# Kernel optimization log

Measured on AMD Instinct MI355X. Metric: run time of the kernel, lower is better.

Reference implementation:

```python
import jax, jax.numpy as jnp
import numpy as np

B, NC, NF, D = 4, 256, 768, 768
TOK_RATIO = 0.5
LN_EPS = 1e-5


def _linear(x, w, b):
    # w: [D_in, D_out]
    return x @ w + b


def _leaky(x):
    return jax.nn.leaky_relu(x, negative_slope=0.01)


def setup_inputs() -> dict:
    key = jax.random.key(0)
    ks = jax.random.split(key, 12)
    s = 1.0 / np.sqrt(D)
    inp = {
        "cls_tokens": jax.random.normal(ks[0], (B, NC, D), dtype=jnp.float32),
        "feats": jax.random.normal(ks[1], (B, NF, D), dtype=jnp.float32),
        "W_head_w": jax.random.uniform(ks[2], (D, D), minval=-s, maxval=s),
        "W_head_b": jax.random.uniform(ks[3], (D,), minval=-s, maxval=s),
        "W_tail_w": jax.random.uniform(ks[4], (D, D), minval=-s, maxval=s),
        "W_tail_b": jax.random.uniform(ks[5], (D,), minval=-s, maxval=s),
        "lin1_w": jax.random.uniform(ks[6], (D, D), minval=-s, maxval=s),
        "lin1_b": jax.random.uniform(ks[7], (D,), minval=-s, maxval=s),
        "lin2_w": jax.random.uniform(ks[8], (D, D), minval=-s, maxval=s),
        "lin2_b": jax.random.uniform(ks[9], (D,), minval=-s, maxval=s),
        "ln_w": jnp.ones((D,), dtype=jnp.float32),
        "ln_b": jnp.zeros((D,), dtype=jnp.float32),
    }
    return inp


def reference(cls_tokens, feats, W_head_w, W_head_b, W_tail_w, W_tail_b,
              lin1_w, lin1_b, lin2_w, lin2_b, ln_w, ln_b):
    topk = int(TOK_RATIO * NC)
    scale = D ** (-0.5)

    # feats is detached in the original (clone().detach())
    x = jnp.concatenate([cls_tokens, jax.lax.stop_gradient(feats)], axis=1)  # [B, Nt, D]

    e_h = _linear(cls_tokens, W_head_w, W_head_b)  # [B, Nc, D]
    e_t = _linear(x, W_tail_w, W_tail_b)           # [B, Nt, D]

    attn_logit = jnp.einsum('bnd,bmd->bnm', e_h * scale, e_t)  # [B, Nc, Nt]
    topk_weight, topk_index = jax.lax.top_k(attn_logit, topk)  # [B, Nc, k]

    # Gather neighbor embeddings: Nb_h[b, n, j] = e_t[b, topk_index[b, n, j]]
    Nb_h = jax.vmap(lambda et, idx: et[idx])(e_t, topk_index)  # [B, Nc, k, D]

    topk_prob = jax.nn.softmax(topk_weight, axis=2)            # [B, Nc, k]
    p = topk_prob[..., None]
    eh_r = p * Nb_h + (1.0 - p) * e_h[:, :, None, :]           # [B, Nc, k, D]

    gate = jnp.tanh(e_h[:, :, None, :] + eh_r)
    ka_weight = jnp.einsum('bnkd,bnkd->bnk', Nb_h, gate)
    ka_prob = jax.nn.softmax(ka_weight, axis=2)
    e_Nh = jnp.einsum('bnk,bnkd->bnd', ka_prob, Nb_h)          # [B, Nc, D]

    # bi-interaction aggregation
    sum_emb = _leaky(_linear((e_h + e_Nh) * 0.1 + cls_tokens, lin1_w, lin1_b))
    bi_emb = _leaky(_linear(e_h * e_Nh * 0.1 + cls_tokens, lin2_w, lin2_b))
    embedding = sum_emb + bi_emb

    # LayerNorm (dropout is a no-op: p=0 and output overwritten in original)
    mu = jnp.mean(embedding, axis=-1, keepdims=True)
    var = jnp.var(embedding, axis=-1, keepdims=True)
    h = (embedding - mu) * jax.lax.rsqrt(var + LN_EPS) * ln_w + ln_b
    return h
```

## Files before the change

kernel.cpp:

```cpp
#include <hip/hip_runtime.h>
#include <hip/hip_bf16.h>
#include <math.h>

#define DDIM 768
#define NCLS 256
#define NFEAT 768
#define NTOK 1024
#define NBATCH 4
#define KSEL 128

typedef float f32x4 __attribute__((ext_vector_type(4)));
typedef short s16x8 __attribute__((ext_vector_type(8)));

__device__ __forceinline__ float wsum(float v) {
#pragma unroll
  for (int o = 32; o; o >>= 1) v += __shfl_down(v, o, 64);
  return v;
}
__device__ __forceinline__ float wmaxr(float v) {
#pragma unroll
  for (int o = 32; o; o >>= 1) v = fmaxf(v, __shfl_down(v, o, 64));
  return v;
}
__device__ __forceinline__ short f2bf(float f) {
  union { __hip_bfloat16 h; short s; } u;
  u.h = __float2bfloat16(f);
  return u.s;
}
__device__ __forceinline__ float bf2f(short s) {
  union { unsigned u; float f; } c;
  c.u = ((unsigned)(unsigned short)s) << 16;
  return c.f;
}
__device__ __forceinline__ void cvt8(float4 x, float4 y, s16x8& h, s16x8& l) {
  float v[8] = {x.x, x.y, x.z, x.w, y.x, y.y, y.z, y.w};
#pragma unroll
  for (int i = 0; i < 8; ++i) {
    short hh = f2bf(v[i]);
    h[i] = hh;
    l[i] = f2bf(v[i] - bf2f(hh));
  }
}
__device__ __forceinline__ int swz(int row, int chunk) {
  return (row << 5) + (((chunk ^ (row >> 1)) & 3) << 3);
}

__global__ __launch_bounds__(256) void prep_all(
    const float* __restrict__ cls, const float* __restrict__ feats,
    const float* __restrict__ w0, const float* __restrict__ w1,
    const float* __restrict__ w2, const float* __restrict__ w3,
    short* __restrict__ h0, short* __restrict__ h1, short* __restrict__ h2,
    short* __restrict__ h3, short* __restrict__ l0, short* __restrict__ l1,
    short* __restrict__ Xh, short* __restrict__ Xl) {
  __shared__ float tile[32][33];
  const int bid = blockIdx.x;
  const int t = threadIdx.x;
  if (bid < 2304) {
    const int z = bid / 576, rem = bid % 576;
    const int by = rem / 24, bx = rem % 24;
    const float* s = z == 0 ? w0 : z == 1 ? w1 : z == 2 ? w2 : w3;
    short* dh = z == 0 ? h0 : z == 1 ? h1 : z == 2 ? h2 : h3;
    short* dl = z == 0 ? l0 : z == 1 ? l1 : nullptr;
    const int tx = t & 31, ty0 = t >> 5;
    const int r0 = by * 32, c0 = bx * 32;
#pragma unroll
    for (int i = 0; i < 4; ++i) {
      int ty = ty0 + i * 8;
      tile[ty][tx] = s[(size_t)(r0 + ty) * DDIM + c0 + tx];
    }
    __syncthreads();
#pragma unroll
    for (int i = 0; i < 4; ++i) {
      int ty = ty0 + i * 8;
      float v = tile[tx][ty];
      short hh = f2bf(v);
      dh[(size_t)(c0 + ty) * DDIM + r0 + tx] = hh;
      if (dl) dl[(size_t)(c0 + ty) * DDIM + r0 + tx] = f2bf(v - bf2f(hh));
    }
  } else {
    const size_t base = ((size_t)(bid - 2304) * 256 + t) * 8;
    const int row = (int)(base / DDIM);
    const int col = (int)(base % DDIM);
    const int b = row >> 10, rr = row & 1023;
    const float* src =
        (rr < NCLS) ? cls + ((size_t)b * NCLS + rr) * DDIM + col
                    : feats + ((size_t)b * NFEAT + (rr - NCLS)) * DDIM + col;
    float4 a0 = *(const float4*)(src);
    float4 a1 = *(const float4*)(src + 4);
    s16x8 h, l;
    cvt8(a0, a1, h, l);
    *(s16x8*)(Xh + base) = h;
    *(s16x8*)(Xl + base) = l;
  }
}

__global__ __launch_bounds__(256) void gemm_front(
    const short* __restrict__ Xh, const short* __restrict__ Xl,
    const short* __restrict__ WhT_h, const short* __restrict__ WhT_l,
    const float* __restrict__ Whb, const short* __restrict__ WtT_h,
    const short* __restrict__ WtT_l, const float* __restrict__ Wtb,
    short* __restrict__ eh_hi, short* __restrict__ eh_lo,
    short* __restrict__ et_hi, short* __restrict__ et_lo) {
  __shared__ short Ah[128 * 32], Al[128 * 32];
  __shared__ short Bh[64 * 32], Bl[64 * 32];
  const int bid = blockIdx.x;
  const int xcd = bid & 7, idx = bid >> 3;
  const int ytile = xcd * 5 + idx / 12;
  const int xtile = idx % 12;
  const int t = threadIdx.x;
  const int row0 = ytile * 128, col0 = xtile * 64;
  const bool head = row0 < 1024;

  const int ar = t >> 1, ac = (t & 1) * 2;
  const int aw0 = swz(ar, ac), aw1 = swz(ar, ac + 1);
  size_t xrow;
  {
    int gr = row0 + ar;
    xrow = head ? (size_t)(((gr >> 8) << 10) + (gr & 255)) : (size_t)(gr - 1024);
  }
  const short* aph = Xh + xrow * DDIM + ac * 8;
  const short* apl = Xl + xrow * DDIM + ac * 8;
  const int br = t >> 2, bc = t & 3;
  const int bw0 = swz(br, bc);
  const short* bph = (head ? WhT_h : WtT_h) + (size_t)(col0 + br) * DDIM + bc * 8;
  const short* bpl = (head ? WhT_l : WtT_l) + (size_t)(col0 + br) * DDIM + bc * 8;
  const float* biasu = head ? Whb : Wtb;

  const int lane = t & 63, wave = t >> 6;
  const int wr = wave >> 1, wc = wave & 1;
  const int fr = lane & 15, fq = lane >> 4;

  f32x4 acc[4][2] = {};
  s16x8 rah0 = *(const s16x8*)(aph);
  s16x8 rah1 = *(const s16x8*)(aph + 8);
  s16x8 ral0 = *(const s16x8*)(apl);
  s16x8 ral1 = *(const s16x8*)(apl + 8);
  s16x8 rbh = *(const s16x8*)(bph);
  s16x8 rbl = *(const s16x8*)(bpl);

  for (int kt = 0; kt < 24; ++kt) {
    __syncthreads();
    *(s16x8*)&Ah[aw0] = rah0;
    *(s16x8*)&Ah[aw1] = rah1;
    *(s16x8*)&Al[aw0] = ral0;
    *(s16x8*)&Al[aw1] = ral1;
    *(s16x8*)&Bh[bw0] = rbh;
    *(s16x8*)&Bl[bw0] = rbl;
    __syncthreads();
    const int kn = (kt < 23 ? kt + 1 : 23) * 32;
    rah0 = *(const s16x8*)(aph + kn);
    rah1 = *(const s16x8*)(aph + kn + 8);
    ral0 = *(const s16x8*)(apl + kn);
    ral1 = *(const s16x8*)(apl + kn + 8);
    rbh = *(const s16x8*)(bph + kn);
    rbl = *(const s16x8*)(bpl + kn);

    s16x8 afh[4], afl[4];
#pragma unroll
    for (int m = 0; m < 4; ++m) {
      int ao = swz(wr * 64 + m * 16 + fr, fq);
      afh[m] = *(const s16x8*)&Ah[ao];
      afl[m] = *(const s16x8*)&Al[ao];
    }
#pragma unroll
    for (int n = 0; n < 2; ++n) {
      int bo = swz(wc * 32 + n * 16 + fr, fq);
      s16x8 bfh = *(const s16x8*)&Bh[bo];
      s16x8 bfl = *(const s16x8*)&Bl[bo];
#pragma unroll
      for (int m = 0; m < 4; ++m) {
        acc[m][n] =
            __builtin_amdgcn_mfma_f32_16x16x32_bf16(afh[m], bfh, acc[m][n], 0, 0, 0);
        acc[m][n] =
            __builtin_amdgcn_mfma_f32_16x16x32_bf16(afh[m], bfl, acc[m][n], 0, 0, 0);
        acc[m][n] =
            __builtin_amdgcn_mfma_f32_16x16x32_bf16(afl[m], bfh, acc[m][n], 0, 0, 0);
      }
    }
  }

  short* Ch = head ? eh_hi : et_hi;
  short* Cl = head ? eh_lo : et_lo;
  const int rbase = head ? row0 : row0 - 1024;
#pragma unroll
  for (int m = 0; m < 4; ++m) {
#pragma unroll
    for (int n = 0; n < 2; ++n) {
#pragma unroll
      for (int r = 0; r < 4; ++r) {
        int rg = rbase + wr * 64 + m * 16 + fq * 4 + r;
        int cg = col0 + wc * 32 + n * 16 + fr;
        float v = acc[m][n][r] + biasu[cg];
        size_t o = (size_t)rg * DDIM + cg;
        short hh = f2bf(v);
        Ch[o] = hh;
        Cl[o] = f2bf(v - bf2f(hh));
      }
    }
  }
}

__global__ __launch_bounds__(256) void gemm_logits(
    const short* __restrict__ eh_hi, const short* __restrict__ eh_lo,
    const short* __restrict__ et_hi, const short* __restrict__ et_lo,
    float* __restrict__ logits, float scale) {
  __shared__ short Ah[32 * 32], Al[32 * 32];
  __shared__ short Bh[64 * 32], Bl[64 * 32];
  const int bid = blockIdx.x;
  const int xcd = bid & 7, idx = bid >> 3;
  const int batch = xcd >> 1;
  const int sub = ((xcd & 1) << 6) | idx;
  const int xtile = sub & 15, ytile = sub >> 4;
  const int row0 = ytile * 32, col0 = xtile * 64;
  const int t = threadIdx.x;

  const int ahalf = t >> 7, ac2 = t & 127;
  const int asr = ac2 >> 2, acc_ = ac2 & 3;
  const short* aptr = (ahalf ? eh_lo : eh_hi) +
                      ((size_t)batch * NCLS + row0 + asr) * DDIM + acc_ * 8;
  const int aso = swz(asr, acc_);
  const int bsr = t >> 2, bcc = t & 3;
  const short* bph = et_hi + ((size_t)batch * NTOK + col0 + bsr) * DDIM + bcc * 8;
  const short* bpl = et_lo + ((size_t)batch * NTOK + col0 + bsr) * DDIM + bcc * 8;
  const int bso = swz(bsr, bcc);

  const int lane = t & 63, wave = t >> 6;
  const int wr = wave >> 1, wc = wave & 1;
  const int fr = lane & 15, fq = lane >> 4;

  f32x4 acc[2] = {};
  s16x8 rA = *(const s16x8*)(aptr);
  s16x8 rbh = *(const s16x8*)(bph);
  s16x8 rbl = *(const s16x8*)(bpl);

  for (int kt = 0; kt < 24; ++kt) {
    __syncthreads();
    *(s16x8*)&(ahalf ? Al : Ah)[aso] = rA;
    *(s16x8*)&Bh[bso] = rbh;
    *(s16x8*)&Bl[bso] = rbl;
    __syncthreads();
    const int kn = (kt < 23 ? kt + 1 : 23) * 32;
    rA = *(const s16x8*)(aptr + kn);
    rbh = *(const s16x8*)(bph + kn);
    rbl = *(const s16x8*)(bpl + kn);
    int ao = swz(wr * 16 + fr, fq);
    s16x8 afh = *(const s16x8*)&Ah[ao];
    s16x8 afl = *(const s16x8*)&Al[ao];
#pragma unroll
    for (int n = 0; n < 2; ++n) {
      int bo = swz(wc * 32 + n * 16 + fr, fq);
      s16x8 bfh = *(const s16x8*)&Bh[bo];
      s16x8 bfl = *(const s16x8*)&Bl[bo];
      acc[n] = __builtin_amdgcn_mfma_f32_16x16x32_bf16(afh, bfh, acc[n], 0, 0, 0);
      acc[n] = __builtin_amdgcn_mfma_f32_16x16x32_bf16(afh, bfl, acc[n], 0, 0, 0);
      acc[n] = __builtin_amdgcn_mfma_f32_16x16x32_bf16(afl, bfh, acc[n], 0, 0, 0);
    }
  }

  float* Cb = logits + (size_t)batch * NCLS * NTOK;
#pragma unroll
  for (int n = 0; n < 2; ++n)
#pragma unroll
    for (int r = 0; r < 4; ++r) {
      int rg = row0 + wr * 16 + fq * 4 + r;
      int cg = col0 + wc * 32 + n * 16 + fr;
      Cb[(size_t)rg * NTOK + cg] = scale * acc[n][r];
    }
}

__global__ __launch_bounds__(256) void select_agg(
    const float* __restrict__ logits, const short* __restrict__ eh_hi,
    const short* __restrict__ et_hi, const float* __restrict__ cls,
    short* __restrict__ inbf) {
  const int bid = blockIdx.x;
  const int xcd = bid & 7, slot = bid >> 3;
  const int batch = xcd >> 1;
  const int row = batch * 256 + (xcd & 1) * 128 + slot;
  const int t = threadIdx.x, lane = t & 63, wave = t >> 6;

  __shared__ int hist[256];
  __shared__ int sh_bin, sh_rem;
  __shared__ int cnt;
  __shared__ int wsumT[4];
  __shared__ float p_sh[KSEL];
  __shared__ int idx_sh[KSEL];
  __shared__ float kaw_sh[KSEL];
  __shared__ float red[2];

  float4 v4 = *(const float4*)(logits + (size_t)row * NTOK + 4 * t);
  float val[4] = {v4.x, v4.y, v4.z, v4.w};
  unsigned key[4];
#pragma unroll
  for (int i = 0; i < 4; ++i) {
    unsigned u = __float_as_uint(val[i]);
    key[i] = (u & 0x80000000u) ? ~u : (u | 0x80000000u);
  }
  unsigned pref = 0, mask = 0;
  int rem = KSEL;
#pragma unroll
  for (int shift = 24; shift >= 0; shift -= 8) {
    hist[t] = 0;
    __syncthreads();
#pragma unroll
    for (int i = 0; i < 4; ++i)
      if ((key[i] & mask) == pref)
        atomicAdd(&hist[(key[i] >> shift) & 255], 1);
    __syncthreads();
    if (wave == 0) {
      int h0 = hist[4 * lane], h1 = hist[4 * lane + 1];
      int h2 = hist[4 * lane + 2], h3 = hist[4 * lane + 3];
      int s = h0 + h1 + h2 + h3;
#pragma unroll
      for (int o = 1; o < 64; o <<= 1) {
        int v = __shfl_down(s, o, 64);
        if (lane + o < 64) s += v;
      }
      int abv = __shfl_down(s, 1, 64);
      if (lane == 63) abv = 0;
      int c3 = abv + h3, c2 = c3 + h2, c1 = c2 + h1, c0 = c1 + h0;
      int bin = -1, nab = 0;
      if (c3 >= rem && abv < rem) { bin = 4 * lane + 3; nab = abv; }
      else if (c2 >= rem && c3 < rem) { bin = 4 * lane + 2; nab = c3; }
      else if (c1 >= rem && c2 < rem) { bin = 4 * lane + 1; nab = c2; }
      else if (c0 >= rem && c1 < rem) { bin = 4 * lane + 0; nab = c1; }
      if (bin >= 0) { sh_bin = bin; sh_rem = rem - nab; }
    }
    __syncthreads();
    pref |= ((unsigned)sh_bin) << shift;
    mask |= 0xFFu << shift;
    rem = sh_rem;
  }
  const unsigned T = pref;
  const int above = KSEL - rem;

  if (t == 0) cnt = 0;
  int tc = 0;
#pragma unroll
  for (int i = 0; i < 4; ++i) tc += (key[i] == T);
  int inc = tc;
#pragma unroll
  for (int o = 1; o < 64; o <<= 1) {
    int v = __shfl_up(inc, o, 64);
    if (lane >= o) inc += v;
  }
  if (lane == 63) wsumT[wave] = inc;
  __syncthreads();
  int wbase = 0;
#pragma unroll
  for (int w = 0; w < 4; ++w)
    if (w < wave) wbase += wsumT[w];
  int excl = wbase + inc - tc;
#pragma unroll
  for (int i = 0; i < 4; ++i) {
    if (key[i] > T) {
      int s2 = atomicAdd(&cnt, 1);
      p_sh[s2] = val[i];
      idx_sh[s2] = 4 * t + i;
    } else if (key[i] == T) {
      int r = excl++;
      if (r < rem) {
        p_sh[above + r] = val[i];
        idx_sh[above + r] = 4 * t + i;
      }
    }
  }
  __syncthreads();

  if (wave == 0) {
    float m = wmaxr(fmaxf(p_sh[lane], p_sh[lane + 64]));
    if (!lane) red[0] = m;
  }
  __syncthreads();
  if (t < KSEL) p_sh[t] = __expf(p_sh[t] - red[0]);
  __syncthreads();
  if (wave == 0) {
    float s = wsum(p_sh[lane] + p_sh[lane + 64]);
    if (!lane) red[1] = s;
  }
  __syncthreads();
  if (t < KSEL) p_sh[t] *= (1.f / red[1]);
  __syncthreads();

  float ehr[12];
  {
    const short* ehrow = eh_hi + (size_t)row * DDIM;
    s16x8 e8 = *(const s16x8*)(ehrow + 8 * lane);
    short4 e4 = *(const short4*)(ehrow + 512 + 4 * lane);
#pragma unroll
    for (int i = 0; i < 8; ++i) ehr[i] = bf2f(e8[i]);
    ehr[8] = bf2f(e4.x);
    ehr[9] = bf2f(e4.y);
    ehr[10] = bf2f(e4.z);
    ehr[11] = bf2f(e4.w);
  }
  const short* etb = et_hi + (size_t)batch * NTOK * DDIM;

  for (int i = 0; i < 32; ++i) {
    int j = wave * 32 + i;
    float pj = p_sh[j];
    float a = 4.f - 2.f * pj, b2 = 2.f * pj;
    const short* nb = etb + (size_t)idx_sh[j] * DDIM;
    s16x8 n8 = *(const s16x8*)(nb + 8 * lane);
    short4 n4 = *(const short4*)(nb + 512 + 4 * lane);
    float nq[12];
#pragma unroll
    for (int q = 0; q < 8; ++q) nq[q] = bf2f(n8[q]);
    nq[8] = bf2f(n4.x);
    nq[9] = bf2f(n4.y);
    nq[10] = bf2f(n4.z);
    nq[11] = bf2f(n4.w);
    float partial = 0.f;
#pragma unroll
    for (int q = 0; q < 12; ++q) {
      float y2 = fmaf(a, ehr[q], b2 * nq[q]);
      float ex = __expf(y2);
      float g = fmaf(-2.f, __builtin_amdgcn_rcpf(1.f + ex), 1.f);
      partial = fmaf(nq[q], g, partial);
    }
    partial = wsum(partial);
    if (!lane) kaw_sh[j] = partial;
  }
  __syncthreads();

  if (wave == 0) {
    float m = wmaxr(fmaxf(kaw_sh[lane], kaw_sh[lane + 64]));
    if (!lane) red[0] = m;
  }
  __syncthreads();
  if (t < KSEL) kaw_sh[t] = __expf(kaw_sh[t] - red[0]);
  __syncthreads();
  if (wave == 0) {
    float s = wsum(kaw_sh[lane] + kaw_sh[lane + 64]);
    if (!lane) red[1] = s;
  }
  __syncthreads();
  if (t < KSEL) kaw_sh[t] *= (1.f / red[1]);
  __syncthreads();

  if (t < 192) {
    const size_t o = (size_t)row * DDIM + 4 * t;
    short4 ehs = *(const short4*)(eh_hi + o);
    float4 eh4 = {bf2f(ehs.x), bf2f(ehs.y), bf2f(ehs.z), bf2f(ehs.w)};
    float4 cl4 = *(const float4*)(cls + o);
    float ax = 0.f, ay = 0.f, az = 0.f, aw = 0.f;
#pragma unroll 8
    for (int j = 0; j < KSEL; ++j) {
      float pr = kaw_sh[j];
      short4 nb = *(const short4*)(etb + (size_t)idx_sh[j] * DDIM + 4 * t);
      ax = fmaf(pr, bf2f(nb.x), ax);
      ay = fmaf(pr, bf2f(nb.y), ay);
      az = fmaf(pr, bf2f(nb.z), az);
      aw = fmaf(pr, bf2f(nb.w), aw);
    }
    short4 sv, bv;
    sv.x = f2bf((eh4.x + ax) * 0.1f + cl4.x);
    sv.y = f2bf((eh4.y + ay) * 0.1f + cl4.y);
    sv.z = f2bf((eh4.z + az) * 0.1f + cl4.z);
    sv.w = f2bf((eh4.w + aw) * 0.1f + cl4.w);
    bv.x = f2bf((eh4.x * ax) * 0.1f + cl4.x);
    bv.y = f2bf((eh4.y * ay) * 0.1f + cl4.y);
    bv.z = f2bf((eh4.z * az) * 0.1f + cl4.z);
    bv.w = f2bf((eh4.w * aw) * 0.1f + cl4.w);
    *(short4*)&inbf[o] = sv;
    *(short4*)&inbf[(size_t)(NBATCH * NCLS) * DDIM + o] = bv;
  }
}

__global__ __launch_bounds__(256) void gemm_lin(
    const short* __restrict__ inbf, const short* __restrict__ L1T,
    const short* __restrict__ L2T, const float* __restrict__ b1,
    const float* __restrict__ b2, float* __restrict__ emb) {
  __shared__ short A1[32 * 32], A2[32 * 32];
  __shared__ short B1[64 * 32], B2[64 * 32];
  const int bid = blockIdx.x;
  const int xcd = bid & 7, idx = bid >> 3;
  const int ytile = xcd * 4 + idx / 12, xtile = idx % 12;
  const int t = threadIdx.x;
  const int row0 = ytile * 32, col0 = xtile * 64;

  const int ahalf = t >> 7, at = t & 127;
  const int asr = at >> 2, asc = at & 3;
  const short* aptr = inbf + (ahalf ? (size_t)1024 * DDIM : 0) +
                      (size_t)(row0 + asr) * DDIM + asc * 8;
  const int aso = swz(asr, asc);
  const int bsr = t >> 2, bsc = t & 3;
  const short* b1p = L1T + (size_t)(col0 + bsr) * DDIM + bsc * 8;
  const short* b2p = L2T + (size_t)(col0 + bsr) * DDIM + bsc * 8;
  const int bso = swz(bsr, bsc);

  const int lane = t & 63, wave = t >> 6;
  const int wr = wave >> 1, wc = wave & 1;
  const int fr = lane & 15, fq = lane >> 4;

  f32x4 acc1[2] = {}, acc2[2] = {};
  s16x8 rA = *(const s16x8*)(aptr);
  s16x8 rB1 = *(const s16x8*)(b1p);
  s16x8 rB2 = *(const s16x8*)(b2p);
  for (int kt = 0; kt < 24; ++kt) {
    __syncthreads();
    *(s16x8*)&(ahalf ? A2 : A1)[aso] = rA;
    *(s16x8*)&B1[bso] = rB1;
    *(s16x8*)&B2[bso] = rB2;
    __syncthreads();
    const int kn = (kt < 23 ? kt + 1 : 23) * 32;
    rA = *(const s16x8*)(aptr + kn);
    rB1 = *(const s16x8*)(b1p + kn);
    rB2 = *(const s16x8*)(b2p + kn);
    int ao = swz(wr * 16 + fr, fq);
    s16x8 a1f = *(const s16x8*)&A1[ao];
    s16x8 a2f = *(const s16x8*)&A2[ao];
#pragma unroll
    for (int n = 0; n < 2; ++n) {
      int bo = swz(wc * 32 + n * 16 + fr, fq);
      s16x8 b1f = *(const s16x8*)&B1[bo];
      s16x8 b2f = *(const s16x8*)&B2[bo];
      acc1[n] = __builtin_amdgcn_mfma_f32_16x16x32_bf16(a1f, b1f, acc1[n], 0, 0, 0);
      acc2[n] = __builtin_amdgcn_mfma_f32_16x16x32_bf16(a2f, b2f, acc2[n], 0, 0, 0);
    }
  }
#pragma unroll
  for (int n = 0; n < 2; ++n)
#pragma unroll
    for (int r = 0; r < 4; ++r) {
      int rg = row0 + wr * 16 + fq * 4 + r;
      int cg = col0 + wc * 32 + n * 16 + fr;
      float v1 = acc1[n][r] + b1[cg];
      v1 = v1 > 0.f ? v1 : 0.01f * v1;
      float v2 = acc2[n][r] + b2[cg];
      v2 = v2 > 0.f ? v2 : 0.01f * v2;
      emb[(size_t)rg * DDIM + cg] = v1 + v2;
    }
}

__global__ __launch_bounds__(256) void ln_kernel(const float* __restrict__ emb,
                                                 const float* __restrict__ lw,
                                                 const float* __restrict__ lb,
                                                 float* __restrict__ out) {
  const int row = blockIdx.x;
  const int t = threadIdx.x;
  const int lane = t & 63, wave = t >> 6;
  __shared__ float red[4];
  __shared__ float bs[2];
  float e[3];
#pragma unroll
  for (int c = 0; c < 3; ++c) e[c] = emb[(size_t)row * DDIM + t + 256 * c];
  float s = e[0] + e[1] + e[2];
  s = wsum(s);
  if (lane == 0) red[wave] = s;
  __syncthreads();
  if (t == 0) bs[0] = (red[0] + red[1] + red[2] + red[3]) * (1.f / DDIM);
  __syncthreads();
  float mu = bs[0];
  float q = 0.f;
#pragma unroll
  for (int c = 0; c < 3; ++c) {
    float d = e[c] - mu;
    q = fmaf(d, d, q);
  }
  q = wsum(q);
  if (lane == 0) red[wave] = q;
  __syncthreads();
  if (t == 0) bs[1] = (red[0] + red[1] + red[2] + red[3]) * (1.f / DDIM);
  __syncthreads();
  float rstd = rsqrtf(bs[1] + 1e-5f);
#pragma unroll
  for (int c = 0; c < 3; ++c) {
    int d = t + 256 * c;
    out[(size_t)row * DDIM + d] = (e[c] - mu) * rstd * lw[d] + lb[d];
  }
}

extern "C" void kernel_launch(void* const* d_in, const int* in_sizes, int n_in,
                              void* d_out, int out_size, void* d_ws,
                              size_t ws_size, hipStream_t stream) {
  const float* cls = (const float*)d_in[0];
  const float* feats = (const float*)d_in[1];
  const float* Whw = (const float*)d_in[2];
  const float* Whb = (const float*)d_in[3];
  const float* Wtw = (const float*)d_in[4];
  const float* Wtb = (const float*)d_in[5];
  const float* l1w = (const float*)d_in[6];
  const float* l1b = (const float*)d_in[7];
  const float* l2w = (const float*)d_in[8];
  const float* l2b = (const float*)d_in[9];
  const float* lnw = (const float*)d_in[10];
  const float* lnb = (const float*)d_in[11];
  float* out = (float*)d_out;

  float* ws = (float*)d_ws;
  float* emb = ws;
  short* eh_hi = (short*)(ws + 3932160);
  short* eh_lo = eh_hi + 786432;
  short* et_hi = (short*)(ws + 4718592);
  short* et_lo = et_hi + 3145728;
  short* WhT_h = (short*)(ws + 7864320);
  short* WhT_l = WhT_h + 589824;
  short* WtT_h = WhT_h + 2 * 589824;
  short* WtT_l = WhT_h + 3 * 589824;
  short* L1T = (short*)(ws + 9043968);
  short* L2T = L1T + 589824;
  float* logits = ws + 7864320;
  short* Xh = (short*)(ws + 9633792);
  short* Xl = Xh + 3145728;
  short* inbf = (short*)(ws + 10027008);
  (void)ws_size;
  (void)in_sizes;
  (void)n_in;
  (void)out_size;

  const float scale = 0.036084391824351615f;
  dim3 blk(256);

  prep_all<<<dim3(3840), blk, 0, stream>>>(cls, feats, Whw, Wtw, l1w, l2w,
                                           WhT_h, WtT_h, L1T, L2T, WhT_l,
                                           WtT_l, Xh, Xl);
  gemm_front<<<dim3(480), blk, 0, stream>>>(
      Xh, Xl, WhT_h, WhT_l, Whb, WtT_h, WtT_l, Wtb, eh_hi, eh_lo, et_hi,
      et_lo);
  gemm_logits<<<dim3(512), blk, 0, stream>>>(eh_hi, eh_lo, et_hi, et_lo,
                                             logits, scale);
  select_agg<<<dim3(1024), blk, 0, stream>>>(logits, eh_hi, et_hi, cls, inbf);
  gemm_lin<<<dim3(384), blk, 0, stream>>>(inbf, L1T, L2T, l1b, l2b, emb);
  ln_kernel<<<dim3(NBATCH * NCLS), blk, 0, stream>>>(emb, lnw, lnb, out);
}
```

Baseline: 118.0 us.

## Double select_agg block to 512 threads and prefetch next neighbor row

Launches the selection/aggregation kernel with 512 threads instead of 256. Each thread now holds 2 logits instead of 4, and each of the 8 waves scores 16 neighbors instead of 32. The neighbor-scoring loop also loads the next neighbor row's bf16 data before computing on the current one, to hide global-memory gather latency. The cost is more register pressure and block-wide syncs across more waves, and the hidden tail of the kernel has to be safe with 512 threads.

Measured after the change: 117.3 us. Within noise of the previous version (-0.6%).

```diff
diff --git a/kernel.cpp b/kernel.cpp
--- a/kernel.cpp
+++ b/kernel.cpp
@@ -268,7 +268,7 @@
     }
 }
 
-__global__ __launch_bounds__(256) void select_agg(
+__global__ __launch_bounds__(512) void select_agg(
     const float* __restrict__ logits, const short* __restrict__ eh_hi,
     const short* __restrict__ et_hi, const float* __restrict__ cls,
     short* __restrict__ inbf) {
@@ -281,17 +281,17 @@
   __shared__ int hist[256];
   __shared__ int sh_bin, sh_rem;
   __shared__ int cnt;
-  __shared__ int wsumT[4];
+  __shared__ int wsumT[8];
   __shared__ float p_sh[KSEL];
   __shared__ int idx_sh[KSEL];
   __shared__ float kaw_sh[KSEL];
   __shared__ float red[2];
 
-  float4 v4 = *(const float4*)(logits + (size_t)row * NTOK + 4 * t);
-  float val[4] = {v4.x, v4.y, v4.z, v4.w};
-  unsigned key[4];
-#pragma unroll
-  for (int i = 0; i < 4; ++i) {
+  float2 v2 = *(const float2*)(logits + (size_t)row * NTOK + 2 * t);
+  float val[2] = {v2.x, v2.y};
+  unsigned key[2];
+#pragma unroll
+  for (int i = 0; i < 2; ++i) {
     unsigned u = __float_as_uint(val[i]);
     key[i] = (u & 0x80000000u) ? ~u : (u | 0x80000000u);
   }
@@ -299,10 +299,10 @@
   int rem = KSEL;
 #pragma unroll
   for (int shift = 24; shift >= 0; shift -= 8) {
-    hist[t] = 0;
-    __syncthreads();
-#pragma unroll
-    for (int i = 0; i < 4; ++i)
+    if (t < 256) hist[t] = 0;
+    __syncthreads();
+#pragma unroll
+    for (int i = 0; i < 2; ++i)
       if ((key[i] & mask) == pref)
         atomicAdd(&hist[(key[i] >> shift) & 255], 1);
     __syncthreads();
@@ -334,9 +334,7 @@
   const int above = KSEL - rem;
 
   if (t == 0) cnt = 0;
-  int tc = 0;
-#pragma unroll
-  for (int i = 0; i < 4; ++i) tc += (key[i] == T);
+  int tc = (key[0] == T) + (key[1] == T);
   int inc = tc;
 #pragma unroll
   for (int o = 1; o < 64; o <<= 1) {
@@ -347,20 +345,20 @@
   __syncthreads();
   int wbase = 0;
 #pragma unroll
-  for (int w = 0; w < 4; ++w)
+  for (int w = 0; w < 8; ++w)
     if (w < wave) wbase += wsumT[w];
   int excl = wbase + inc - tc;
 #pragma unroll
-  for (int i = 0; i < 4; ++i) {
+  for (int i = 0; i < 2; ++i) {
     if (key[i] > T) {
       int s2 = atomicAdd(&cnt, 1);
       p_sh[s2] = val[i];
-      idx_sh[s2] = 4 * t + i;
+      idx_sh[s2] = 2 * t + i;
     } else if (key[i] == T) {
       int r = excl++;
       if (r < rem) {
         p_sh[above + r] = val[i];
-        idx_sh[above + r] = 4 * t + i;
+        idx_sh[above + r] = 2 * t + i;
       }
     }
   }
@@ -395,30 +393,42 @@
   }
   const short* etb = et_hi + (size_t)batch * NTOK * DDIM;
 
-  for (int i = 0; i < 32; ++i) {
-    int j = wave * 32 + i;
-    float pj = p_sh[j];
-    float a = 4.f - 2.f * pj, b2 = 2.f * pj;
-    const short* nb = etb + (size_t)idx_sh[j] * DDIM;
-    s16x8 n8 = *(const s16x8*)(nb + 8 * lane);
-    short4 n4 = *(const short4*)(nb + 512 + 4 * lane);
-    float nq[12];
-#pragma unroll
-    for (int q = 0; q < 8; ++q) nq[q] = bf2f(n8[q]);
-    nq[8] = bf2f(n4.x);
-    nq[9] = bf2f(n4.y);
-    nq[10] = bf2f(n4.z);
-    nq[11] = bf2f(n4.w);
-    float partial = 0.f;
-#pragma unroll
-    for (int q = 0; q < 12; ++q) {
-      float y2 = fmaf(a, ehr[q], b2 * nq[q]);
-      float ex = __expf(y2);
-      float g = fmaf(-2.f, __builtin_amdgcn_rcpf(1.f + ex), 1.f);
-      partial = fmaf(nq[q], g, partial);
-    }
-    partial = wsum(partial);
-    if (!lane) kaw_sh[j] = partial;
+  {
+    const int jb = wave * 16;
+    const short* nb0 = etb + (size_t)idx_sh[jb] * DDIM;
+    s16x8 n8 = *(const s16x8*)(nb0 + 8 * lane);
+    short4 n4 = *(const short4*)(nb0 + 512 + 4 * lane);
+    for (int i = 0; i < 16; ++i) {
+      const int j = jb + i;
+      s16x8 n8n;
+      short4 n4n;
+      if (i < 15) {
+        const short* nbn = etb + (size_t)idx_sh[j + 1] * DDIM;
+        n8n = *(const s16x8*)(nbn + 8 * lane);
+        n4n = *(const short4*)(nbn + 512 + 4 * lane);
+      }
+      float pj = p_sh[j];
+      float a = 4.f - 2.f * pj, b2 = 2.f * pj;
+      float nq[12];
+#pragma unroll
+      for (int q = 0; q < 8; ++q) nq[q] = bf2f(n8[q]);
+      nq[8] = bf2f(n4.x);
+      nq[9] = bf2f(n4.y);
+      nq[10] = bf2f(n4.z);
+      nq[11] = bf2f(n4.w);
+      float partial = 0.f;
+#pragma unroll
+      for (int q = 0; q < 12; ++q) {
+        float y2 = fmaf(a, ehr[q], b2 * nq[q]);
+        float ex = __expf(y2);
+        float g = fmaf(-2.f, __builtin_amdgcn_rcpf(1.f + ex), 1.f);
+        partial = fmaf(nq[q], g, partial);
+      }
+      partial = wsum(partial);
+      if (!lane) kaw_sh[j] = partial;
+      n8 = n8n;
+      n4 = n4n;
+    }
   }
   __syncthreads();
 
@@ -619,7 +629,8 @@
       et_lo);
   gemm_logits<<<dim3(512), blk, 0, stream>>>(eh_hi, eh_lo, et_hi, et_lo,
                                              logits, scale);
-  select_agg<<<dim3(1024), blk, 0, stream>>>(logits, eh_hi, et_hi, cls, inbf);
+  select_agg<<<dim3(1024), dim3(512), 0, stream>>>(logits, eh_hi, et_hi, cls,
+                                                   inbf);
   gemm_lin<<<dim3(384), blk, 0, stream>>>(inbf, L1T, L2T, l1b, l2b, emb);
   ln_kernel<<<dim3(NBATCH * NCLS), blk, 0, stream>>>(emb, lnw, lnb, out);
 }
```
